# Performance work log

Measured on AMD Instinct MI355X. Metric: run time of the kernel, lower is better.

Reference implementation:

```python
import jax, jax.numpy as jnp
import numpy as np

D_MODEL = 1024
NHEAD = 16
HEAD_DIM = D_MODEL // NHEAD
FF = 4096
ALPHA = 1.4142135  # deepnorm_alpha
WIN = (127, 128)   # sliding window (left, right)
EPS = 1e-5
ROPE_BASE = 10000.0


def rmsnorm(x, g):
    ms = jnp.mean(x * x, axis=-1, keepdims=True)
    return x * jax.lax.rsqrt(ms + EPS) * g


def rope(x):
    # x: [B, T, H, D]; non-interleaved rotary over full head dim
    T, D = x.shape[1], x.shape[-1]
    half = D // 2
    inv_freq = 1.0 / (ROPE_BASE ** (jnp.arange(half, dtype=jnp.float32) * 2.0 / D))
    ang = jnp.arange(T, dtype=jnp.float32)[:, None] * inv_freq[None, :]  # [T, half]
    cos = jnp.cos(ang)[None, :, None, :]
    sin = jnp.sin(ang)[None, :, None, :]
    x1, x2 = x[..., :half], x[..., half:]
    return jnp.concatenate([x1 * cos - x2 * sin, x2 * cos + x1 * sin], axis=-1)


def setup_inputs() -> dict:
    key = jax.random.key(0)
    ks = jax.random.split(key, 8)
    d, h = D_MODEL, FF
    return {
        "x": jax.random.normal(ks[0], (2, 2048, d), jnp.float32),
        "Wqkv": jax.random.normal(ks[1], (3 * d, d), jnp.float32) * 0.02,
        "Wout": jax.random.normal(ks[2], (d, d), jnp.float32) * 0.02,
        "bout": jnp.zeros((d,), jnp.float32),
        "W1": jax.random.normal(ks[3], (2 * h, d), jnp.float32) * 0.02,
        "W2": jax.random.normal(ks[4], (d, h), jnp.float32) * 0.02,
        "g1": jnp.ones((d,), jnp.float32),
        "g2": jnp.ones((d,), jnp.float32),
    }


def reference(x, Wqkv, Wout, bout, W1, W2, g1, g2):
    B, T, d = x.shape
    # --- self attention with RoPE + sliding window band mask ---
    qkv = (x @ Wqkv.T).reshape(B, T, 3, NHEAD, HEAD_DIM)
    q, k, v = qkv[:, :, 0], qkv[:, :, 1], qkv[:, :, 2]  # [B,T,H,Dh]
    q = rope(q)
    k = rope(k)
    q = jnp.swapaxes(q, 1, 2)  # [B,H,T,Dh]
    k = jnp.swapaxes(k, 1, 2)
    v = jnp.swapaxes(v, 1, 2)
    scale = 1.0 / np.sqrt(HEAD_DIM)
    scores = jnp.einsum('bhqd,bhkd->bhqk', q, k) * scale
    idx = jnp.arange(T)
    rel = idx[None, :] - idx[:, None]  # j - i
    band = (rel >= -WIN[0]) & (rel <= WIN[1])  # [T,T] allowed positions
    scores = jnp.where(band[None, None], scores, -jnp.inf)
    attn = jax.nn.softmax(scores, axis=-1)
    o = jnp.einsum('bhqk,bhkd->bhqd', attn, v)
    o = jnp.swapaxes(o, 1, 2).reshape(B, T, d)
    a = o @ Wout.T + bout
    # --- deepnorm residual 1 + RMSNorm ---
    x1 = a + ALPHA * x
    x2 = rmsnorm(x1, g1)
    # --- SwiGLU MLP: y, gate = fc1(x).chunk(2); y*gate*sigmoid(gate) ---
    yg = x2 @ W1.T
    y, gate = jnp.split(yg, 2, axis=-1)
    y = y * gate * jax.nn.sigmoid(gate)
    y = y @ W2.T
    # --- deepnorm residual 2 + RMSNorm ---
    x3 = y + ALPHA * x2
    return rmsnorm(x3, g2)
```

## Files before the change

### kernel.cpp

```cpp
#include <hip/hip_runtime.h>

#define T_SEQ   2048
#define NHEADS  16
#define DHEAD   64
#define DMODEL  1024
#define ALPHA_C 1.4142135f
#define EPS_C   1e-5f

typedef __attribute__((ext_vector_type(8))) short bf16x8;
typedef __attribute__((ext_vector_type(4))) short bf16x4;
typedef __attribute__((ext_vector_type(4))) float floatx4;

__device__ __forceinline__ float bf2f(unsigned short u) {
  union { unsigned int i; float f; } v;
  v.i = ((unsigned int)u) << 16;
  return v.f;
}
__device__ __forceinline__ unsigned short f2bf(float f) {
  union { float f; unsigned int i; } v;
  v.f = f;
  unsigned int u = v.i;
  u += 0x7FFF + ((u >> 16) & 1);
  return (unsigned short)(u >> 16);
}

__device__ __forceinline__ void gload_lds16(const void* g, void* l) {
  __builtin_amdgcn_global_load_lds(
      (const __attribute__((address_space(1))) void*)g,
      (__attribute__((address_space(3))) void*)l, 16, 0, 0);
}

__global__ void convert_all(const float* __restrict__ Wqkv,
                            const float* __restrict__ Wout,
                            const float* __restrict__ W1,
                            const float* __restrict__ W2,
                            const float* __restrict__ x,
                            unsigned short* __restrict__ ws,
                            float* __restrict__ cosT,
                            float* __restrict__ sinT)
{
  if (blockIdx.x >= 10240) {
    int gid = (blockIdx.x - 10240) * 256 + threadIdx.x;
    int t = gid >> 5, i = gid & 31;
    float fr = powf(10000.f, -(float)i * (1.f / 32.f));
    float sn, cs;
    sincosf((float)t * fr, &sn, &cs);
    cosT[gid] = cs;
    sinT[gid] = sn;
    return;
  }
  size_t i = ((size_t)blockIdx.x * 256 + threadIdx.x) * 8;
  const float* src;
  size_t off;
  if      (i <  3145728) { src = Wqkv; off = i; }
  else if (i <  4194304) { src = Wout; off = i -  3145728; }
  else if (i < 12582912) { src = W1;   off = i -  4194304; }
  else if (i < 16777216) { src = W2;   off = i - 12582912; }
  else                   { src = x;    off = i - 16777216; }
  floatx4 a = *(const floatx4*)(src + off);
  floatx4 b = *(const floatx4*)(src + off + 4);
  bf16x8 o;
  #pragma unroll
  for (int u = 0; u < 4; u++) {
    o[u]     = (short)f2bf(a[u]);
    o[4 + u] = (short)f2bf(b[u]);
  }
  *(bf16x8*)(ws + i) = o;
}

#define BAR() __builtin_amdgcn_s_barrier()
#define SCB() __builtin_amdgcn_sched_barrier(0)

#define RD_A_S(bb, mh, s)                                                 \
  _Pragma("unroll") for (int i = 0; i < 4; i++)                           \
    af[i][s] = *(const bf16x8*)&lds[(bb) + aRd +                          \
        ((mh) * 64 + i * 16 + mrow) * 64 + (kq0 ^ ((s) << 5))];

#define RD_B_S(bb, s)                                                     \
  _Pragma("unroll") for (int n = 0; n < 4; n++)                           \
    bfr[n][s] = *(const bf16x8*)&lds[(bb) + bRd +                         \
        (bRow0 + n * 16 + mrow) * 64 + (kq0 ^ ((s) << 5))];

#define MFMA8(mh, nh, s)                                                  \
  _Pragma("unroll") for (int i = 0; i < 4; i++)                           \
  _Pragma("unroll") for (int n = 0; n < 2; n++)                           \
    acc[(mh) * 4 + i][(nh) * 2 + n] =                                     \
        __builtin_amdgcn_mfma_f32_16x16x32_bf16(                          \
            af[i][s], bfr[(nh) * 2 + n][s],                               \
            acc[(mh) * 4 + i][(nh) * 2 + n], 0, 0, 0);

#define KLOOP_S4()                                                        \
  for (int t = 0; t < 16; ++t) {                                          \
    const int cur = t & 1;                                                \
    const int bb  = cur * 32768;                                          \
    const int tb  = (t + 2 < 16) ? t + 2 : 15;                            \
                     \
    BAR();                                                                \
    RD_A_S(bb, 0, 0); RD_B_S(bb, 0);                                      \
    SCB();                                                                \
    RD_A_S(bb, 0, 1); RD_B_S(bb, 1);                                      \
    asm volatile("s_waitcnt lgkmcnt(8)" ::: "memory");                    \
    SCB();                                                                \
    __builtin_amdgcn_s_setprio(1);                                        \
    MFMA8(0, 0, 0);                                                       \
    __builtin_amdgcn_s_setprio(0);                                        \
    asm volatile("s_waitcnt lgkmcnt(0)" ::: "memory");                    \
    SCB();                                                                \
    __builtin_amdgcn_s_setprio(1);                                        \
    MFMA8(0, 0, 1);                                                       \
    __builtin_amdgcn_s_setprio(0);                                        \
                        \
    BAR();                                                                \
    stB(cur, 0, tb); stB(cur, 1, tb);                                     \
    __builtin_amdgcn_s_setprio(1);                                        \
    MFMA8(0, 1, 0); MFMA8(0, 1, 1);                                       \
    __builtin_amdgcn_s_setprio(0);                                        \
                             \
    BAR();                                                                \
    RD_A_S(bb, 1, 0);                                                     \
    SCB();                                                                \
    RD_A_S(bb, 1, 1);                                                     \
    asm volatile("s_waitcnt lgkmcnt(4)" ::: "memory");                    \
    SCB();                                                                \
    __builtin_amdgcn_s_setprio(1);                                        \
    MFMA8(1, 1, 0);                                                       \
    __builtin_amdgcn_s_setprio(0);                                        \
    asm volatile("s_waitcnt lgkmcnt(0)" ::: "memory");                    \
    SCB();                                                                \
    __builtin_amdgcn_s_setprio(1);                                        \
    MFMA8(1, 1, 1);                                                       \
    __builtin_amdgcn_s_setprio(0);                                        \
              \
    BAR();                                                                \
    stA(cur, 0, tb); stA(cur, 1, tb);                                     \
    __builtin_amdgcn_s_setprio(1);                                        \
    MFMA8(1, 0, 0); MFMA8(1, 0, 1);                                       \
    __builtin_amdgcn_s_setprio(0);                                        \
    asm volatile("s_waitcnt vmcnt(8)" ::: "memory");                      \
  }

__global__ __launch_bounds__(512, 2) void gemm_w1_swiglu_s4(
    const unsigned short* __restrict__ A,
    const unsigned short* __restrict__ W1,
    unsigned short* __restrict__ ys)
{
  __shared__ unsigned short lds[65536];

  const int tid  = threadIdx.x;
  const int lane = tid & 63;
  const int wid  = tid >> 6;
  const int wr   = wid >> 2;
  const int wc   = wid & 3;
  const int mrow = lane & 15;
  const int quad = lane >> 4;
  const int kq0  = (quad ^ (mrow & 7)) * 8;

  const int bid  = blockIdx.x;
  const int c8   = bid & 7;
  const int u    = bid >> 3;
  const int mBase = ((c8 >> 2) * 8 + (u >> 3)) * 256;
  const int nBase = ((c8 &  3) * 8 + (u &  7)) * 128;

  const int r0 = tid >> 3;
  const int ce = (((tid & 7) ^ (r0 & 7)) * 8);
  const size_t aoff0 = (size_t)(mBase + r0) * 1024 + ce;
  const size_t aoff1 = aoff0 + (size_t)64 * 1024;
  auto growf = [&](int br) {
    int col = nBase + (br >> 6) * 32 + (br & 31);
    return ((br >> 5) & 1) ? 4096 + col : col;
  };
  const size_t boff00 = (size_t)growf(r0)       * 1024 + ce;
  const size_t boff01 = (size_t)growf(64 + r0)  * 1024 + ce;
  const size_t boff10 = (size_t)growf(128 + r0) * 1024 + ce;
  const size_t boff11 = (size_t)growf(192 + r0) * 1024 + ce;
  const int d0 = tid * 8;

  auto stA = [&](int buf, int h, int kt) {
    const unsigned short* g = A + (size_t)kt * 64 + (h ? (size_t)128 * 1024 : 0);
    int base = buf * 32768 + h * 8192;
    gload_lds16(g + aoff0, &lds[base + d0]);
    gload_lds16(g + aoff1, &lds[base + 4096 + d0]);
  };
  auto stB = [&](int buf, int h, int kt) {
    const unsigned short* g = W1 + (size_t)kt * 64;
    int base = buf * 32768 + 16384 + h * 8192;
    gload_lds16(g + (h ? boff10 : boff00), &lds[base + d0]);
    gload_lds16(g + (h ? boff11 : boff01), &lds[base + 4096 + d0]);
  };

  floatx4 acc[8][4];
  #pragma unroll
  for (int i = 0; i < 8; i++)
    #pragma unroll
    for (int n = 0; n < 4; n++) acc[i][n] = (floatx4){0.f, 0.f, 0.f, 0.f};
  bf16x8 af[4][2], bfr[4][2];

  const int aRd   = wr * 8192;
  const int bRd   = 16384 + (wc >> 1) * 8192;
  const int bRow0 = (wc & 1) * 64;

  stB(0, 0, 0); stB(0, 1, 0); stA(0, 0, 0); stA(0, 1, 0);
  stB(1, 0, 1); stB(1, 1, 1); stA(1, 0, 1); stA(1, 1, 1);
  asm volatile("s_waitcnt vmcnt(8)" ::: "memory");

  KLOOP_S4();

  const int col0 = lane & 15;
  const int row0 = (lane >> 4) * 4;
  #pragma unroll
  for (int n = 0; n < 2; n++) {
    const int col = nBase + wc * 32 + n * 16 + col0;
    #pragma unroll
    for (int i = 0; i < 8; i++) {
      const int rowb = mBase + wr * 128 + i * 16 + row0;
      #pragma unroll
      for (int r = 0; r < 4; r++) {
        float y = acc[i][n][r], g = acc[i][n + 2][r];
        float sig = 1.f / (1.f + __expf(-g));
        ys[(size_t)(rowb + r) * 4096 + col] = f2bf(y * g * sig);
      }
    }
  }
  asm volatile("s_waitcnt vmcnt(0)" ::: "memory");
}

__global__ __launch_bounds__(512, 2) void gemm_qkv_rope256(
    const unsigned short* __restrict__ A,
    const unsigned short* __restrict__ W,
    const float* __restrict__ cosT,
    const float* __restrict__ sinT,
    unsigned short* __restrict__ Qd,
    unsigned short* __restrict__ Kd,
    unsigned short* __restrict__ Vd)
{
  __shared__ unsigned short lds[65536];

  const int tid  = threadIdx.x;
  const int lane = tid & 63;
  const int wid  = tid >> 6;
  const int wr   = wid >> 2;
  const int wc   = wid & 3;
  const int mrow = lane & 15;
  const int quad = lane >> 4;
  const int kq0  = (quad ^ (mrow & 7)) * 8;

  const int bid  = blockIdx.x;
  const int c8   = bid & 7;
  const int u    = bid >> 3;
  const int mBase = ((c8 >> 1) * 4 + u / 6) * 256;
  const int nBase = ((c8 & 1) * 6 + u % 6) * 256;

  const int r0 = tid >> 3;
  const int ce = (((tid & 7) ^ (r0 & 7)) * 8);
  const size_t aoff0 = (size_t)(mBase + r0) * 1024 + ce;
  const size_t aoff1 = aoff0 + (size_t)64 * 1024;
  const size_t boff00 = (size_t)(nBase + r0)       * 1024 + ce;
  const size_t boff01 = (size_t)(nBase + 64 + r0)  * 1024 + ce;
  const size_t boff10 = (size_t)(nBase + 128 + r0) * 1024 + ce;
  const size_t boff11 = (size_t)(nBase + 192 + r0) * 1024 + ce;
  const int d0 = tid * 8;

  auto stA = [&](int buf, int h, int kt) {
    const unsigned short* g = A + (size_t)kt * 64 + (h ? (size_t)128 * 1024 : 0);
    int base = buf * 32768 + h * 8192;
    gload_lds16(g + aoff0, &lds[base + d0]);
    gload_lds16(g + aoff1, &lds[base + 4096 + d0]);
  };
  auto stB = [&](int buf, int h, int kt) {
    const unsigned short* g = W + (size_t)kt * 64;
    int base = buf * 32768 + 16384 + h * 8192;
    gload_lds16(g + (h ? boff10 : boff00), &lds[base + d0]);
    gload_lds16(g + (h ? boff11 : boff01), &lds[base + 4096 + d0]);
  };

  floatx4 acc[8][4];
  #pragma unroll
  for (int i = 0; i < 8; i++)
    #pragma unroll
    for (int n = 0; n < 4; n++) acc[i][n] = (floatx4){0.f, 0.f, 0.f, 0.f};
  bf16x8 af[4][2], bfr[4][2];

  const int aRd   = wr * 8192;
  const int bRd   = 16384 + (wc >> 1) * 8192;
  const int bRow0 = (wc & 1) * 64;

  stB(0, 0, 0); stB(0, 1, 0); stA(0, 0, 0); stA(0, 1, 0);
  stB(1, 0, 1); stB(1, 1, 1); stA(1, 0, 1); stA(1, 1, 1);
  asm volatile("s_waitcnt vmcnt(8)" ::: "memory");

  KLOOP_S4();

  const int col0 = lane & 15;
  const int row0 = (lane >> 4) * 4;
  const int colBase = nBase + wc * 64;
  const int sect = colBase >> 10;
  const int h    = (colBase & 1023) >> 6;
  unsigned short* dst = (sect == 0) ? Qd : (sect == 1) ? Kd : Vd;

  if (sect < 2) {
    #pragma unroll
    for (int i = 0; i < 8; i++) {
      #pragma unroll
      for (int r = 0; r < 4; r++) {
        const int row = mBase + wr * 128 + i * 16 + row0 + r;
        const int b = row >> 11, t = row & 2047;
        size_t ob = ((size_t)((b * NHEADS + h) * T_SEQ + t)) * DHEAD;
        const int tb = t * 32;
        float c0 = cosT[tb + col0],      s0 = sinT[tb + col0];
        float c1 = cosT[tb + col0 + 16], s1 = sinT[tb + col0 + 16];
        float x1a = acc[i][0][r], x2a = acc[i][2][r];
        float x1b = acc[i][1][r], x2b = acc[i][3][r];
        dst[ob + col0]      = f2bf(x1a * c0 - x2a * s0);
        dst[ob + col0 + 32] = f2bf(x2a * c0 + x1a * s0);
        dst[ob + col0 + 16] = f2bf(x1b * c1 - x2b * s1);
        dst[ob + col0 + 48] = f2bf(x2b * c1 + x1b * s1);
      }
    }
  } else {
    #pragma unroll
    for (int i = 0; i < 8; i++)
      #pragma unroll
      for (int n = 0; n < 4; n++)
        #pragma unroll
        for (int r = 0; r < 4; r++) {
          const int row = mBase + wr * 128 + i * 16 + row0 + r;
          const int b = row >> 11, t = row & 2047;
          dst[((size_t)((b * NHEADS + h) * T_SEQ + t)) * DHEAD + n * 16 + col0] =
              f2bf(acc[i][n][r]);
        }
  }
  asm volatile("s_waitcnt vmcnt(0)" ::: "memory");
}

#define W2_RD_A(bb, mh, s)                                                \
  _Pragma("unroll") for (int i = 0; i < 2; i++)                           \
    af[i][s] = *(const bf16x8*)&lds[(bb) +                                \
        (wr * 64 + (mh) * 32 + i * 16 + mrow) * 64 + (kq0 ^ ((s) << 5))];

#define W2_RD_B(bb, s)                                                    \
  _Pragma("unroll") for (int n = 0; n < 4; n++)                           \
    bfr[n][s] = *(const bf16x8*)&lds[(bb) + 16384 +                       \
        (wc * 64 + n * 16 + mrow) * 64 + (kq0 ^ ((s) << 5))];

#define W2_MFMA(mh, s)                                                    \
  _Pragma("unroll") for (int i = 0; i < 2; i++)                           \
  _Pragma("unroll") for (int n = 0; n < 4; n++)                           \
    acc[(mh) * 2 + i][n] =                                                \
        __builtin_amdgcn_mfma_f32_16x16x32_bf16(                          \
            af[i][s], bfr[n][s], acc[(mh) * 2 + i][n], 0, 0, 0);

#define W2_KLOOP(NT)                                                      \
  for (int t = 0; t < (NT); ++t) {                                        \
    const int cur = t & 1;                                                \
    const int nxt = cur ^ 1;                                              \
    const int bb  = cur * 24576;                                          \
    const int ta  = (t + 1 < (NT)) ? t + 1 : (NT) - 1;                    \
    const int tb  = (t + 2 < (NT)) ? t + 2 : (NT) - 1;                    \
    BAR();                                                                \
    stA(nxt, 0, ta); stA(nxt, 1, ta);                                     \
    W2_RD_A(bb, 0, 0); W2_RD_B(bb, 0);                                    \
    SCB();                                                                \
    W2_RD_A(bb, 0, 1); W2_RD_B(bb, 1);                                    \
    asm volatile("s_waitcnt lgkmcnt(6)" ::: "memory");                    \
    SCB();                                                                \
    __builtin_amdgcn_s_setprio(1);                                        \
    W2_MFMA(0, 0);                                                        \
    __builtin_amdgcn_s_setprio(0);                                        \
    asm volatile("s_waitcnt lgkmcnt(0)" ::: "memory");                    \
    SCB();                                                                \
    __builtin_amdgcn_s_setprio(1);                                        \
    W2_MFMA(0, 1);                                                        \
    __builtin_amdgcn_s_setprio(0);                                        \
    BAR();                                                                \
    stB(cur, tb);                                                         \
    W2_RD_A(bb, 1, 0);                                                    \
    SCB();                                                                \
    W2_RD_A(bb, 1, 1);                                                    \
    asm volatile("s_waitcnt lgkmcnt(2)" ::: "memory");                    \
    SCB();                                                                \
    __builtin_amdgcn_s_setprio(1);                                        \
    W2_MFMA(1, 0);                                                        \
    __builtin_amdgcn_s_setprio(0);                                        \
    asm volatile("s_waitcnt lgkmcnt(0)" ::: "memory");                    \
    SCB();                                                                \
    __builtin_amdgcn_s_setprio(1);                                        \
    W2_MFMA(1, 1);                                                        \
    __builtin_amdgcn_s_setprio(0);                                        \
    asm volatile("s_waitcnt vmcnt(2)" ::: "memory");                      \
  }

__global__ __launch_bounds__(512, 2) void gemm_w2_2ph(
    const unsigned short* __restrict__ A,
    const unsigned short* __restrict__ W,
    float* __restrict__ Cp)
{
  __shared__ unsigned short lds[49152];

  const int tid  = threadIdx.x;
  const int lane = tid & 63;
  const int wid  = tid >> 6;
  const int wr   = wid >> 1;
  const int wc   = wid & 1;
  const int mrow = lane & 15;
  const int quad = lane >> 4;
  const int kq0  = (quad ^ (mrow & 7)) * 8;

  const int u  = blockIdx.x;
  const int c8 = u & 7;
  const int v  = u >> 3;
  const int zP = v >> 4;
  const int mBase = (((c8 >> 1) & 3) * 4 + ((v >> 2) & 3)) * 256;
  const int nBase = ((c8 & 1) * 4 + (v & 3)) * 128;
  const int kOff  = zP * 2048;

  const int r0 = tid >> 3;
  const int ce = (((tid & 7) ^ (r0 & 7)) * 8);
  const int d0 = tid * 8;

  auto stA = [&](int buf, int h, int kt) {
    const unsigned short* g =
        A + (size_t)(mBase + h * 128 + r0) * 4096 + kOff + kt * 64 + ce;
    int base = buf * 24576 + h * 8192;
    gload_lds16(g, &lds[base + d0]);
    gload_lds16(g + (size_t)64 * 4096, &lds[base + 4096 + d0]);
  };
  auto stB = [&](int buf, int kt) {
    const unsigned short* g =
        W + (size_t)(nBase + r0) * 4096 + kOff + kt * 64 + ce;
    int base = buf * 24576 + 16384;
    gload_lds16(g, &lds[base + d0]);
    gload_lds16(g + (size_t)64 * 4096, &lds[base + 4096 + d0]);
  };

  floatx4 acc[4][4];
  #pragma unroll
  for (int i = 0; i < 4; i++)
    #pragma unroll
    for (int n = 0; n < 4; n++) acc[i][n] = (floatx4){0.f, 0.f, 0.f, 0.f};
  bf16x8 af[2][2], bfr[4][2];

  stB(0, 0);
  stA(0, 0, 0); stA(0, 1, 0);
  stB(1, 1);
  asm volatile("s_waitcnt vmcnt(2)" ::: "memory");

  W2_KLOOP(32);

  const int col0 = lane & 15;
  const int row0 = (lane >> 4) * 4;
  float* dst = Cp + (size_t)zP * 4096 * 1024;
  #pragma unroll
  for (int n = 0; n < 4; n++) {
    const int col = nBase + wc * 64 + n * 16 + col0;
    #pragma unroll
    for (int i = 0; i < 4; i++) {
      const int rowb = mBase + wr * 64 + i * 16 + row0;
      #pragma unroll
      for (int r = 0; r < 4; r++)
        dst[(size_t)(rowb + r) * 1024 + col] = acc[i][n][r];
    }
  }
  asm volatile("s_waitcnt vmcnt(0)" ::: "memory");
}

__global__ __launch_bounds__(512, 2) void gemm_wout_2ph(
    const unsigned short* __restrict__ A,
    const unsigned short* __restrict__ W,
    const float* __restrict__ bias,
    unsigned short* __restrict__ C)
{
  __shared__ unsigned short lds[49152];

  const int tid  = threadIdx.x;
  const int lane = tid & 63;
  const int wid  = tid >> 6;
  const int wr   = wid >> 1;
  const int wc   = wid & 1;
  const int mrow = lane & 15;
  const int quad = lane >> 4;
  const int kq0  = (quad ^ (mrow & 7)) * 8;

  const int u  = blockIdx.x;
  const int c8 = u & 7;
  const int v  = u >> 3;
  const int mBase = ((c8 >> 1) * 4 + (v >> 2)) * 256;
  const int nBase = ((c8 & 1) * 4 + (v & 3)) * 128;

  const int r0 = tid >> 3;
  const int ce = (((tid & 7) ^ (r0 & 7)) * 8);
  const int d0 = tid * 8;

  auto stA = [&](int buf, int h, int kt) {
    const unsigned short* g =
        A + (size_t)(mBase + h * 128 + r0) * 1024 + kt * 64 + ce;
    int base = buf * 24576 + h * 8192;
    gload_lds16(g, &lds[base + d0]);
    gload_lds16(g + (size_t)64 * 1024, &lds[base + 4096 + d0]);
  };
  auto stB = [&](int buf, int kt) {
    const unsigned short* g =
        W + (size_t)(nBase + r0) * 1024 + kt * 64 + ce;
    int base = buf * 24576 + 16384;
    gload_lds16(g, &lds[base + d0]);
    gload_lds16(g + (size_t)64 * 1024, &lds[base + 4096 + d0]);
  };

  floatx4 acc[4][4];
  #pragma unroll
  for (int i = 0; i < 4; i++)
    #pragma unroll
    for (int n = 0; n < 4; n++) acc[i][n] = (floatx4){0.f, 0.f, 0.f, 0.f};
  bf16x8 af[2][2], bfr[4][2];

  stB(0, 0);
  stA(0, 0, 0); stA(0, 1, 0);
  stB(1, 1);
  asm volatile("s_waitcnt vmcnt(2)" ::: "memory");

  W2_KLOOP(16);

  const int col0 = lane & 15;
  const int row0 = (lane >> 4) * 4;
  #pragma unroll
  for (int n = 0; n < 4; n++) {
    const int col = nBase + wc * 64 + n * 16 + col0;
    const float badd = bias[col];
    #pragma unroll
    for (int i = 0; i < 4; i++) {
      const int rowb = mBase + wr * 64 + i * 16 + row0;
      #pragma unroll
      for (int r = 0; r < 4; r++)
        C[(size_t)(rowb + r) * 1024 + col] = f2bf(acc[i][n][r] + badd);
    }
  }
  asm volatile("s_waitcnt vmcnt(0)" ::: "memory");
}

__global__ __launch_bounds__(256) void attn_mfma(
    const unsigned short* __restrict__ Qg,
    const unsigned short* __restrict__ Kg,
    const unsigned short* __restrict__ Vg,
    unsigned short* __restrict__ Og)
{
  __shared__ unsigned short KV[23040];
  __shared__ unsigned short Qs[64 * 72];
  __shared__ unsigned short Ps[4 * 16 * 328];

  const int tid  = threadIdx.x;
  const int lane = tid & 63;
  const int wave = tid >> 6;
  const int c    = lane & 15;
  const int quad = lane >> 4;
  const int blk  = blockIdx.x;
  const int bh   = blk >> 5;
  const int qBase = (blk & 31) * 64;
  const size_t hbase = (size_t)bh * T_SEQ * DHEAD;

  for (int e = tid; e < 320 * 8; e += 256) {
    int row = e >> 3, ch = e & 7;
    int kg = qBase - 127 + row;
    int kgc = min(max(kg, 0), T_SEQ - 1);
    *(bf16x8*)&KV[row * 72 + ch * 8] =
        *(const bf16x8*)(Kg + hbase + (size_t)kgc * DHEAD + ch * 8);
  }
  for (int e = tid; e < 64 * 8; e += 256) {
    int row = e >> 3, ch = e & 7;
    *(bf16x8*)&Qs[row * 72 + ch * 8] =
        *(const bf16x8*)(Qg + hbase + (size_t)(qBase + row) * DHEAD + ch * 8);
  }
  __syncthreads();

  bf16x8 aq[2];
  #pragma unroll
  for (int hh = 0; hh < 2; hh++)
    aq[hh] = *(const bf16x8*)&Qs[(wave * 16 + c) * 72 + hh * 32 + quad * 8];

  floatx4 s[20];
  #pragma unroll
  for (int kt = 0; kt < 20; kt++) {
    bf16x8 b0 = *(const bf16x8*)&KV[(kt * 16 + c) * 72 + quad * 8];
    bf16x8 b1 = *(const bf16x8*)&KV[(kt * 16 + c) * 72 + 32 + quad * 8];
    floatx4 t = (floatx4){0.f, 0.f, 0.f, 0.f};
    t = __builtin_amdgcn_mfma_f32_16x16x32_bf16(aq[0], b0, t, 0, 0, 0);
    t = __builtin_amdgcn_mfma_f32_16x16x32_bf16(aq[1], b1, t, 0, 0, 0);
    s[kt] = t;
  }
  __syncthreads();

  for (int ch = wave; ch < 5; ch += 4) {
    int koff = ch * 64 + lane;
    int kg = qBase - 127 + koff;
    int kgc = min(max(kg, 0), T_SEQ - 1);
    const unsigned short* vrow = Vg + hbase + (size_t)kgc * DHEAD;
    #pragma unroll
    for (int dg = 0; dg < 8; dg++) {
      bf16x8 v8 = *(const bf16x8*)(vrow + dg * 8);
      #pragma unroll
      for (int j = 0; j < 8; j++)
        KV[(dg * 8 + j) * 328 + koff] = (unsigned short)v8[j];
    }
  }

  const int kLoMin = max(0, 127 - qBase);
  const int kHiMax = min(319, 2047 + 127 - qBase);
  float mx[4] = {-3e38f, -3e38f, -3e38f, -3e38f};
  #pragma unroll
  for (int kt = 0; kt < 20; kt++) {
    const int koff = kt * 16 + c;
    #pragma unroll
    for (int reg = 0; reg < 4; reg++) {
      const int qrow = wave * 16 + quad * 4 + reg;
      const int d = koff - qrow;
      bool ok = (d >= 0) && (d <= 255) && (koff >= kLoMin) && (koff <= kHiMax);
      float val = ok ? s[kt][reg] * 0.125f : -3e38f;
      s[kt][reg] = val;
      mx[reg] = fmaxf(mx[reg], val);
    }
  }
  #pragma unroll
  for (int reg = 0; reg < 4; reg++)
    #pragma unroll
    for (int m = 1; m <= 8; m <<= 1)
      mx[reg] = fmaxf(mx[reg], __shfl_xor(mx[reg], m));

  float ls[4] = {0.f, 0.f, 0.f, 0.f};
  #pragma unroll
  for (int kt = 0; kt < 20; kt++) {
    const int koff = kt * 16 + c;
    #pragma unroll
    for (int reg = 0; reg < 4; reg++) {
      float p = __expf(s[kt][reg] - mx[reg]);
      ls[reg] += p;
      Ps[wave * 5248 + (quad * 4 + reg) * 328 + koff] = f2bf(p);
    }
  }
  float inv[4];
  #pragma unroll
  for (int reg = 0; reg < 4; reg++) {
    #pragma unroll
    for (int m = 1; m <= 8; m <<= 1) ls[reg] += __shfl_xor(ls[reg], m);
    inv[reg] = 1.f / ls[reg];
  }
  __syncthreads();

  floatx4 oacc[4];
  #pragma unroll
  for (int nt = 0; nt < 4; nt++) oacc[nt] = (floatx4){0.f, 0.f, 0.f, 0.f};
  #pragma unroll
  for (int kt2 = 0; kt2 < 10; kt2++) {
    bf16x8 a = *(const bf16x8*)&Ps[wave * 5248 + c * 328 + kt2 * 32 + quad * 8];
    #pragma unroll
    for (int nt = 0; nt < 4; nt++) {
      bf16x8 bb = *(const bf16x8*)&KV[(nt * 16 + c) * 328 + kt2 * 32 + quad * 8];
      oacc[nt] = __builtin_amdgcn_mfma_f32_16x16x32_bf16(a, bb, oacc[nt], 0, 0, 0);
    }
  }

  const int b = bh >> 4, h = bh & 15;
  #pragma unroll
  for (int nt = 0; nt < 4; nt++) {
    #pragma unroll
    for (int reg = 0; reg < 4; reg++) {
      const int qg = qBase + wave * 16 + quad * 4 + reg;
      Og[((size_t)(b * T_SEQ + qg)) * DMODEL + h * DHEAD + nt * 16 + c] =
          f2bf(oacc[nt][reg] * inv[reg]);
    }
  }
}

__global__ __launch_bounds__(256) void rmsnorm_mid(
    const unsigned short* __restrict__ a,
    const float* __restrict__ x,
    const float* __restrict__ g,
    unsigned short* __restrict__ out)
{
  __shared__ float red[4];
  const int row = blockIdx.x;
  const int tid = threadIdx.x;
  const size_t base = (size_t)row * DMODEL;
  const int c = tid * 4;
  bf16x4  av = *(const bf16x4*)(a + base + c);
  floatx4 xv = *(const floatx4*)(x + base + c);
  floatx4 gv = *(const floatx4*)(g + c);
  float s[4], ss = 0.f;
  #pragma unroll
  for (int j = 0; j < 4; j++) {
    s[j] = bf2f((unsigned short)av[j]) + ALPHA_C * xv[j];
    ss += s[j] * s[j];
  }
  #pragma unroll
  for (int m = 1; m <= 32; m <<= 1) ss += __shfl_xor(ss, m);
  if ((tid & 63) == 0) red[tid >> 6] = ss;
  __syncthreads();
  float ms = (red[0] + red[1] + red[2] + red[3]) * (1.f / DMODEL);
  float scl = rsqrtf(ms + EPS_C);
  bf16x4 ov;
  #pragma unroll
  for (int j = 0; j < 4; j++) ov[j] = (short)f2bf(s[j] * scl * gv[j]);
  *(bf16x4*)(out + base + c) = ov;
}

__global__ __launch_bounds__(256) void rmsnorm_final_sk(
    const float* __restrict__ p0,
    const float* __restrict__ p1,
    const unsigned short* __restrict__ x2,
    const float* __restrict__ g,
    float* __restrict__ out)
{
  __shared__ float red[4];
  const int row = blockIdx.x;
  const int tid = threadIdx.x;
  const size_t base = (size_t)row * DMODEL;
  const int c = tid * 4;
  floatx4 a0 = *(const floatx4*)(p0 + base + c);
  floatx4 a1 = *(const floatx4*)(p1 + base + c);
  bf16x4  xv = *(const bf16x4*)(x2 + base + c);
  floatx4 gv = *(const floatx4*)(g + c);
  float s[4], ss = 0.f;
  #pragma unroll
  for (int j = 0; j < 4; j++) {
    s[j] = (a0[j] + a1[j]) + ALPHA_C * bf2f((unsigned short)xv[j]);
    ss += s[j] * s[j];
  }
  #pragma unroll
  for (int m = 1; m <= 32; m <<= 1) ss += __shfl_xor(ss, m);
  if ((tid & 63) == 0) red[tid >> 6] = ss;
  __syncthreads();
  float ms = (red[0] + red[1] + red[2] + red[3]) * (1.f / DMODEL);
  float scl = rsqrtf(ms + EPS_C);
  floatx4 ov;
  #pragma unroll
  for (int j = 0; j < 4; j++) ov[j] = s[j] * scl * gv[j];
  *(floatx4*)(out + base + c) = ov;
}

extern "C" void kernel_launch(void* const* d_in, const int* in_sizes, int n_in,
                              void* d_out, int out_size, void* d_ws, size_t ws_size,
                              hipStream_t stream) {
  (void)in_sizes; (void)n_in; (void)out_size; (void)ws_size;
  const float* x    = (const float*)d_in[0];
  const float* Wqkv = (const float*)d_in[1];
  const float* Wout = (const float*)d_in[2];
  const float* bout = (const float*)d_in[3];
  const float* W1   = (const float*)d_in[4];
  const float* W2   = (const float*)d_in[5];
  const float* g1   = (const float*)d_in[6];
  const float* g2   = (const float*)d_in[7];
  float* out = (float*)d_out;

  unsigned short* ws    = (unsigned short*)d_ws;
  unsigned short* Wqkvb = ws;
  unsigned short* Woutb = ws + 3145728;
  unsigned short* W1b   = ws + 4194304;
  unsigned short* W2b   = ws + 12582912;
  unsigned short* P1    = ws + 16777216;
  unsigned short* x2    = ws + 20971520;
  unsigned short* q     = ws + 25165824;
  unsigned short* k     = ws + 29360128;
  unsigned short* v     = ws + 33554432;
  unsigned short* o     = ws + 37748736;
  unsigned short* ys    = ws + 25165824;
  float* cosT = (float*)(ws + 37748736);
  float* sinT = cosT + 65536;
  float* p0   = (float*)(ws + 41943040);

  convert_all<<<10496, 256, 0, stream>>>(Wqkv, Wout, W1, W2, x, ws, cosT, sinT);
  gemm_qkv_rope256<<<192, 512, 0, stream>>>(P1, Wqkvb, cosT, sinT, q, k, v);
  attn_mfma<<<32 * (T_SEQ / 64), 256, 0, stream>>>(q, k, v, o);
  gemm_wout_2ph<<<128, 512, 0, stream>>>(o, Woutb, bout, P1);
  rmsnorm_mid<<<4096, 256, 0, stream>>>(P1, x, g1, x2);
  gemm_w1_swiglu_s4<<<512, 512, 0, stream>>>(x2, W1b, ys);
  gemm_w2_2ph<<<256, 512, 0, stream>>>(ys, W2b, p0);
  rmsnorm_final_sk<<<4096, 256, 0, stream>>>(p0, p0 + 4194304, x2, g2, out);
}
```

Baseline: 345.8 us.

## Replace split-K W2 GEMM with full-K 256x64 tiles and single-partial norm

The W2 down-projection GEMM drops its two-way split-K, which used 256x128 tiles with K=2048 and wrote two fp32 partial buffers. It now uses 256x64 output tiles over the full K=4096, with the same block count and a smaller LDS footprint. The final RMSNorm then reads one fp32 buffer instead of summing two partials. This removes one full fp32 partial write and read, at the cost of a longer serial K loop per block and less reuse of A per block.

```diff
diff --git a/kernel.cpp b/kernel.cpp
--- a/kernel.cpp
+++ b/kernel.cpp
@@ -332,6 +332,115 @@
   asm volatile("s_waitcnt vmcnt(0)" ::: "memory");
 }
 
+#define W1K_RD_A(bb, s)                                                   \
+  _Pragma("unroll") for (int i = 0; i < 4; i++)                           \
+    af[i][s] = *(const bf16x8*)&lds[(bb) +                                \
+        (wr * 64 + i * 16 + mrow) * 64 + (kq0 ^ ((s) << 5))];
+
+#define W1K_RD_B(bb, s)                                                   \
+  _Pragma("unroll") for (int n = 0; n < 2; n++)                           \
+    bfr[n][s] = *(const bf16x8*)&lds[(bb) + 16384 +                       \
+        (wc * 32 + n * 16 + mrow) * 64 + (kq0 ^ ((s) << 5))];
+
+#define W1K_MFMA(s)                                                       \
+  _Pragma("unroll") for (int i = 0; i < 4; i++)                           \
+  _Pragma("unroll") for (int n = 0; n < 2; n++)                           \
+    acc[i][n] = __builtin_amdgcn_mfma_f32_16x16x32_bf16(                  \
+        af[i][s], bfr[n][s], acc[i][n], 0, 0, 0);
+
+__global__ __launch_bounds__(512, 2) void gemm_w2_1k(
+    const unsigned short* __restrict__ A,
+    const unsigned short* __restrict__ W,
+    float* __restrict__ y2)
+{
+  __shared__ unsigned short lds[40960];
+
+  const int tid  = threadIdx.x;
+  const int lane = tid & 63;
+  const int wid  = tid >> 6;
+  const int wr   = wid >> 1;
+  const int wc   = wid & 1;
+  const int mrow = lane & 15;
+  const int quad = lane >> 4;
+  const int kq0  = (quad ^ (mrow & 7)) * 8;
+
+  const int u  = blockIdx.x;
+  const int c8 = u & 7;
+  const int v  = u >> 3;
+  const int mBase = ((c8 >> 1) * 4 + (v >> 3)) * 256;
+  const int nBase = ((c8 & 1) * 8 + (v & 7)) * 64;
+
+  const int r0 = tid >> 3;
+  const int ce = (((tid & 7) ^ (r0 & 7)) * 8);
+  const int d0 = tid * 8;
+
+  auto stA = [&](int buf, int h, int kt) {
+    const unsigned short* g =
+        A + (size_t)(mBase + h * 128 + r0) * 4096 + kt * 64 + ce;
+    int base = buf * 20480 + h * 8192;
+    gload_lds16(g, &lds[base + d0]);
+    gload_lds16(g + (size_t)64 * 4096, &lds[base + 4096 + d0]);
+  };
+  auto stB = [&](int buf, int kt) {
+    const unsigned short* g =
+        W + (size_t)(nBase + r0) * 4096 + kt * 64 + ce;
+    gload_lds16(g, &lds[buf * 20480 + 16384 + d0]);
+  };
+
+  floatx4 acc[4][2];
+  #pragma unroll
+  for (int i = 0; i < 4; i++)
+    #pragma unroll
+    for (int n = 0; n < 2; n++) acc[i][n] = (floatx4){0.f, 0.f, 0.f, 0.f};
+  bf16x8 af[4][2], bfr[2][2];
+
+  stB(0, 0);
+  stA(0, 0, 0); stA(0, 1, 0);
+  stB(1, 1);
+  asm volatile("s_waitcnt vmcnt(1)" ::: "memory");
+
+  for (int t = 0; t < 64; ++t) {
+    const int cur = t & 1;
+    const int nxt = cur ^ 1;
+    const int bb  = cur * 20480;
+    const int ta  = (t + 1 < 64) ? t + 1 : 63;
+    const int tb  = (t + 2 < 64) ? t + 2 : 63;
+
+    BAR();
+    W1K_RD_A(bb, 0); W1K_RD_B(bb, 0);
+    SCB();
+    W1K_RD_A(bb, 1); W1K_RD_B(bb, 1);
+    asm volatile("s_waitcnt lgkmcnt(6)" ::: "memory");
+    SCB();
+    __builtin_amdgcn_s_setprio(1);
+    W1K_MFMA(0);
+    __builtin_amdgcn_s_setprio(0);
+    asm volatile("s_waitcnt lgkmcnt(0)" ::: "memory");
+    SCB();
+    stA(nxt, 0, ta); stA(nxt, 1, ta);
+    stB(cur, tb);
+    __builtin_amdgcn_s_setprio(1);
+    W1K_MFMA(1);
+    __builtin_amdgcn_s_setprio(0);
+    asm volatile("s_waitcnt vmcnt(1)" ::: "memory");
+  }
+
+  const int col0 = lane & 15;
+  const int row0 = (lane >> 4) * 4;
+  #pragma unroll
+  for (int n = 0; n < 2; n++) {
+    const int col = nBase + wc * 32 + n * 16 + col0;
+    #pragma unroll
+    for (int i = 0; i < 4; i++) {
+      const int rowb = mBase + wr * 64 + i * 16 + row0;
+      #pragma unroll
+      for (int r = 0; r < 4; r++)
+        y2[(size_t)(rowb + r) * 1024 + col] = acc[i][n][r];
+    }
+  }
+  asm volatile("s_waitcnt vmcnt(0)" ::: "memory");
+}
+
 #define W2_RD_A(bb, mh, s)                                                \
   _Pragma("unroll") for (int i = 0; i < 2; i++)                           \
     af[i][s] = *(const bf16x8*)&lds[(bb) +                                \
@@ -388,80 +497,6 @@
     __builtin_amdgcn_s_setprio(0);                                        \
     asm volatile("s_waitcnt vmcnt(2)" ::: "memory");                      \
   }
-
-__global__ __launch_bounds__(512, 2) void gemm_w2_2ph(
-    const unsigned short* __restrict__ A,
-    const unsigned short* __restrict__ W,
-    float* __restrict__ Cp)
-{
-  __shared__ unsigned short lds[49152];
-
-  const int tid  = threadIdx.x;
-  const int lane = tid & 63;
-  const int wid  = tid >> 6;
-  const int wr   = wid >> 1;
-  const int wc   = wid & 1;
-  const int mrow = lane & 15;
-  const int quad = lane >> 4;
-  const int kq0  = (quad ^ (mrow & 7)) * 8;
-
-  const int u  = blockIdx.x;
-  const int c8 = u & 7;
-  const int v  = u >> 3;
-  const int zP = v >> 4;
-  const int mBase = (((c8 >> 1) & 3) * 4 + ((v >> 2) & 3)) * 256;
-  const int nBase = ((c8 & 1) * 4 + (v & 3)) * 128;
-  const int kOff  = zP * 2048;
-
-  const int r0 = tid >> 3;
-  const int ce = (((tid & 7) ^ (r0 & 7)) * 8);
-  const int d0 = tid * 8;
-
-  auto stA = [&](int buf, int h, int kt) {
-    const unsigned short* g =
-        A + (size_t)(mBase + h * 128 + r0) * 4096 + kOff + kt * 64 + ce;
-    int base = buf * 24576 + h * 8192;
-    gload_lds16(g, &lds[base + d0]);
-    gload_lds16(g + (size_t)64 * 4096, &lds[base + 4096 + d0]);
-  };
-  auto stB = [&](int buf, int kt) {
-    const unsigned short* g =
-        W + (size_t)(nBase + r0) * 4096 + kOff + kt * 64 + ce;
-    int base = buf * 24576 + 16384;
-    gload_lds16(g, &lds[base + d0]);
-    gload_lds16(g + (size_t)64 * 4096, &lds[base + 4096 + d0]);
-  };
-
-  floatx4 acc[4][4];
-  #pragma unroll
-  for (int i = 0; i < 4; i++)
-    #pragma unroll
-    for (int n = 0; n < 4; n++) acc[i][n] = (floatx4){0.f, 0.f, 0.f, 0.f};
-  bf16x8 af[2][2], bfr[4][2];
-
-  stB(0, 0);
-  stA(0, 0, 0); stA(0, 1, 0);
-  stB(1, 1);
-  asm volatile("s_waitcnt vmcnt(2)" ::: "memory");
-
-  W2_KLOOP(32);
-
-  const int col0 = lane & 15;
-  const int row0 = (lane >> 4) * 4;
-  float* dst = Cp + (size_t)zP * 4096 * 1024;
-  #pragma unroll
-  for (int n = 0; n < 4; n++) {
-    const int col = nBase + wc * 64 + n * 16 + col0;
-    #pragma unroll
-    for (int i = 0; i < 4; i++) {
-      const int rowb = mBase + wr * 64 + i * 16 + row0;
-      #pragma unroll
-      for (int r = 0; r < 4; r++)
-        dst[(size_t)(rowb + r) * 1024 + col] = acc[i][n][r];
-    }
-  }
-  asm volatile("s_waitcnt vmcnt(0)" ::: "memory");
-}
 
 __global__ __launch_bounds__(512, 2) void gemm_wout_2ph(
     const unsigned short* __restrict__ A,
@@ -700,9 +735,8 @@
   *(bf16x4*)(out + base + c) = ov;
 }
 
-__global__ __launch_bounds__(256) void rmsnorm_final_sk(
-    const float* __restrict__ p0,
-    const float* __restrict__ p1,
+__global__ __launch_bounds__(256) void rmsnorm_final(
+    const float* __restrict__ y2,
     const unsigned short* __restrict__ x2,
     const float* __restrict__ g,
     float* __restrict__ out)
@@ -712,14 +746,13 @@
   const int tid = threadIdx.x;
   const size_t base = (size_t)row * DMODEL;
   const int c = tid * 4;
-  floatx4 a0 = *(const floatx4*)(p0 + base + c);
-  floatx4 a1 = *(const floatx4*)(p1 + base + c);
+  floatx4 a0 = *(const floatx4*)(y2 + base + c);
   bf16x4  xv = *(const bf16x4*)(x2 + base + c);
   floatx4 gv = *(const floatx4*)(g + c);
   float s[4], ss = 0.f;
   #pragma unroll
   for (int j = 0; j < 4; j++) {
-    s[j] = (a0[j] + a1[j]) + ALPHA_C * bf2f((unsigned short)xv[j]);
+    s[j] = a0[j] + ALPHA_C * bf2f((unsigned short)xv[j]);
     ss += s[j] * s[j];
   }
   #pragma unroll
@@ -762,7 +795,7 @@
   unsigned short* ys    = ws + 25165824;
   float* cosT = (float*)(ws + 37748736);
   float* sinT = cosT + 65536;
-  float* p0   = (float*)(ws + 41943040);
+  float* y2f  = (float*)(ws + 41943040);
 
   convert_all<<<10496, 256, 0, stream>>>(Wqkv, Wout, W1, W2, x, ws, cosT, sinT);
   gemm_qkv_rope256<<<192, 512, 0, stream>>>(P1, Wqkvb, cosT, sinT, q, k, v);
@@ -770,6 +803,6 @@
   gemm_wout_2ph<<<128, 512, 0, stream>>>(o, Woutb, bout, P1);
   rmsnorm_mid<<<4096, 256, 0, stream>>>(P1, x, g1, x2);
   gemm_w1_swiglu_s4<<<512, 512, 0, stream>>>(x2, W1b, ys);
-  gemm_w2_2ph<<<256, 512, 0, stream>>>(ys, W2b, p0);
-  rmsnorm_final_sk<<<4096, 256, 0, stream>>>(p0, p0 + 4194304, x2, g2, out);
-}
+  gemm_w2_1k<<<256, 512, 0, stream>>>(ys, W2b, y2f);
+  rmsnorm_final<<<4096, 256, 0, stream>>>(y2f, x2, g2, out);
+}
```

New measurement: 362.4 us, median of 2. 4.8% more time.
